# Performance work log

Measured on AMD Instinct MI355X. Metric: run time of the kernel, lower is better.

The kernel has to match this reference:

```python
import jax, jax.numpy as jnp
import numpy as np

N, E, H = 2000, 4096, 256

def setup_inputs() -> dict:
    key = jax.random.key(0)
    ks = jax.random.split(key, 24)
    def rn(k, shape, scale=0.05):
        return jax.random.normal(k, shape, dtype=jnp.float32) * scale
    inp = {
        'x': jax.random.randint(ks[0], (N, 1), 0, 5),
        'pos': rn(ks[1], (N, 3), 1.0),
        'edge_index': jax.random.randint(ks[2], (2, E), 0, N),
        'edge_atr': rn(ks[3], (E, 5), 1.0),
        'emb_table': rn(ks[4], (5, 5), 1.0),
        'lin0_W': rn(ks[5], (H, 8)), 'lin0_b': jnp.zeros((H,), jnp.float32),
        'mlp1_W': rn(ks[6], (128, 5)), 'mlp1_b': jnp.zeros((128,), jnp.float32),
        'mlp2_W': rn(ks[7], (H * H, 128), 0.01), 'mlp2_b': jnp.zeros((H * H,), jnp.float32),
        'conv_b': jnp.zeros((H,), jnp.float32),
        'gru_Wih': rn(ks[8], (3 * H, H)), 'gru_Whh': rn(ks[9], (3 * H, H)),
        'gru_bih': jnp.zeros((3 * H,), jnp.float32), 'gru_bhh': jnp.zeros((3 * H,), jnp.float32),
        'lin1_W': rn(ks[10], (H, 2 * H)), 'lin1_b': jnp.zeros((H,), jnp.float32),
        'lin2_W': rn(ks[11], (242, H)), 'lin2_b': jnp.zeros((242,), jnp.float32),
        'l6_W1': rn(ks[12], (128, 2 * H)), 'l6_b1': jnp.zeros((128,), jnp.float32),
        'bn_g': jnp.ones((128,), jnp.float32), 'bn_b': jnp.zeros((128,), jnp.float32),
        'l6_W2': rn(ks[13], (1, 128)), 'l6_b2': jnp.zeros((1,), jnp.float32),
    }
    return inp

def _gru_step(m, h, Wih, Whh, bih, bhh):
    gi = m @ Wih.T + bih  # [N,3H]
    gh = h @ Whh.T + bhh
    gir, giz, gin = jnp.split(gi, 3, axis=1)
    ghr, ghz, ghn = jnp.split(gh, 3, axis=1)
    r = jax.nn.sigmoid(gir + ghr)
    z = jax.nn.sigmoid(giz + ghz)
    n = jnp.tanh(gin + r * ghn)
    return (1.0 - z) * n + z * h

def reference(x, pos, edge_index, edge_atr, emb_table, lin0_W, lin0_b,
              mlp1_W, mlp1_b, mlp2_W, mlp2_b, conv_b,
              gru_Wih, gru_Whh, gru_bih, gru_bhh,
              lin1_W, lin1_b, lin2_W, lin2_b,
              l6_W1, l6_b1, bn_g, bn_b, l6_W2, l6_b2):
    node_emb = emb_table[x[:, 0]]                      # [N,5]
    in_p = jnp.concatenate([node_emb, pos], axis=1)    # [N,8]
    out = jax.nn.relu(in_p @ lin0_W.T + lin0_b)        # [N,H]
    h = out
    row, col = edge_index[0], edge_index[1]
    # edge-conditioned weights (edge_atr is loop-invariant -> compute once)
    he = jax.nn.relu(edge_atr @ mlp1_W.T + mlp1_b)     # [E,128]
    W_e = (he @ mlp2_W.T + mlp2_b).reshape(E, H, H)    # [E,H,H]
    counts = jnp.clip(jax.ops.segment_sum(jnp.ones((E,), jnp.float32), col, num_segments=N), 1.0)
    for _ in range(3):
        msg = jnp.einsum('eh,eho->eo', out[row], W_e)  # gather + per-edge matmul
        agg = jax.ops.segment_sum(msg, col, num_segments=N) / counts[:, None] + conv_b
        m = jax.nn.relu(agg)
        h = _gru_step(m, h, gru_Wih, gru_Whh, gru_bih, gru_bhh)
        out = h
    out_concat = jnp.concatenate([out[row], out[col]], axis=1)  # [E,2H]
    o1 = jax.nn.relu(out_concat @ lin1_W.T + lin1_b)
    out2 = o1 @ lin2_W.T + lin2_b                       # [E,242]
    # lin6: Linear -> BatchNorm1d (batch stats, training mode) -> ReLU -> Linear
    h1 = out_concat @ l6_W1.T + l6_b1                   # [E,128]
    mu = jnp.mean(h1, axis=0)
    var = jnp.var(h1, axis=0)
    h1n = (h1 - mu) * jax.lax.rsqrt(var + 1e-5) * bn_g + bn_b
    precs = jax.nn.relu(h1n) @ l6_W2.T + l6_b2          # [E,1]
    return (out2, precs)
```

## Files before the change

kernel.cpp:

```cpp
#include <hip/hip_runtime.h>
#include <hip/hip_bf16.h>

constexpr int N_ = 2000;
constexpr int E_ = 4096;
constexpr int H_ = 256;
constexpr int KH_ = 128;
constexpr int NV_ = H_ * KH_;
constexpr int MPAD_ = 2048;
constexpr int NG_ = 768;
constexpr float VSCALE = 64.f;
constexpr float VSCALE_INV = 1.f / 64.f;

typedef short bf16x8 __attribute__((ext_vector_type(8)));
typedef float f32x4  __attribute__((ext_vector_type(4)));
typedef float f32x2  __attribute__((ext_vector_type(2)));

__device__ __forceinline__ float bf_lo(unsigned u) { return __uint_as_float(u << 16); }
__device__ __forceinline__ float bf_hi(unsigned u) { return __uint_as_float(u & 0xffff0000u); }
__device__ __forceinline__ short bfbits(float f) {
    __hip_bfloat16 b = __float2bfloat16(f);
    return *(short*)&b;
}

#define PIPE_WAIT_ENTER(N_OUTST)                                   \
    asm volatile("s_waitcnt vmcnt(" #N_OUTST ")" ::: "memory");    \
    __builtin_amdgcn_s_barrier();                                  \
    asm volatile("" ::: "memory");                                 \
    __builtin_amdgcn_sched_barrier(0);

#define PIPE_EXIT()                                                \
    __builtin_amdgcn_sched_barrier(0);                             \
    asm volatile("" ::: "memory");                                 \
    __builtin_amdgcn_s_barrier();

__global__ void k_lin0(const int* __restrict__ x, const float* __restrict__ pos,
                       const float* __restrict__ emb, const float* __restrict__ W,
                       const float* __restrict__ b, float* __restrict__ out,
                       __hip_bfloat16* __restrict__ Abf) {
    int n = blockIdx.x, t = threadIdx.x;
    if (n >= N_) { Abf[(size_t)n * H_ + t] = __float2bfloat16(0.f); return; }
    __shared__ float in_p[8];
    if (t < 5) in_p[t] = emb[x[n] * 5 + t];
    else if (t < 8) in_p[t] = pos[n * 3 + (t - 5)];
    __syncthreads();
    float acc = b[t];
#pragma unroll
    for (int i = 0; i < 8; i++) acc += in_p[i] * W[t * 8 + i];
    float v = fmaxf(acc, 0.f);
    out[n * H_ + t] = v;
    Abf[(size_t)n * H_ + t] = __float2bfloat16(v);
}

__global__ void k_he(const float* __restrict__ ea, const float* __restrict__ W,
                     const float* __restrict__ b, float* __restrict__ he) {
    int e = blockIdx.x, t = threadIdx.x;
    __shared__ float a[5];
    if (t < 5) a[t] = ea[e * 5 + t];
    __syncthreads();
    float acc = b[t];
#pragma unroll
    for (int i = 0; i < 5; i++) acc += a[i] * W[t * 5 + i];
    he[e * KH_ + t] = fmaxf(acc, 0.f);
}

__global__ void k_counts(const int* __restrict__ ei, float* __restrict__ counts) {
    int e = blockIdx.x * blockDim.x + threadIdx.x;
    if (e < E_) atomicAdd(&counts[ei[E_ + e]], 1.0f);
}

__global__ void k_trans_bt(const float* __restrict__ W, __hip_bfloat16* __restrict__ Bt) {
    __shared__ float tile[32][68];
    int t = threadIdx.x;
    int n0 = blockIdx.x * 64, k0 = blockIdx.y * 32;
#pragma unroll
    for (int i = 0; i < 2; i++) {
        int idx = t + i * 256;
        int kk = idx >> 4, nn = (idx & 15) * 4;
        float4 f = *(const float4*)&W[(size_t)(k0 + kk) * NV_ + n0 + nn];
        *(float4*)&tile[kk][nn] = f;
    }
    __syncthreads();
#pragma unroll
    for (int i = 0; i < 2; i++) {
        int idx = t + i * 256;
        int nn = idx >> 3, k4 = (idx & 7) * 4;
        short4 s;
        s.x = bfbits(tile[k4 + 0][nn]);
        s.y = bfbits(tile[k4 + 1][nn]);
        s.z = bfbits(tile[k4 + 2][nn]);
        s.w = bfbits(tile[k4 + 3][nn]);
        *(short4*)&Bt[(size_t)(n0 + nn) * H_ + k0 + k4] = s;
    }
}

__global__ void k_prep_w(const float* __restrict__ Wih, const float* __restrict__ Whh,
                         const float* __restrict__ lin1W, const float* __restrict__ l6W1,
                         const float* __restrict__ lin2W, const float* __restrict__ b2,
                         __hip_bfloat16* __restrict__ WihB, __hip_bfloat16* __restrict__ WhhB,
                         __hip_bfloat16* __restrict__ Bpk,
                         __hip_bfloat16* __restrict__ lin2Wb, __hip_bfloat16* __restrict__ BtB) {
    int i = blockIdx.x * 256 + threadIdx.x;
    if (i < NG_ * H_) {
        WihB[i] = __float2bfloat16(Wih[i]);
        WhhB[i] = __float2bfloat16(Whh[i]);
    }
    Bpk[i] = __float2bfloat16(i < 256 * 512 ? lin1W[i] : l6W1[i - 256 * 512]);
    if (i < 128 * 2 * H_) {
        int r = i >> 8, k = i & 255;
        lin2Wb[i] = __float2bfloat16(r < 242 ? lin2W[r * H_ + k] : 0.f);
        int o = i >> 8, h = i & 255;
        BtB[o * H_ + h] = __float2bfloat16(b2[h * H_ + o]);
    }
}

template <int KD, bool RELU, bool OUT_BF16>
__global__ __launch_bounds__(256, 3) void k_gemm_nt(const __hip_bfloat16* __restrict__ A,
                                                    const __hip_bfloat16* __restrict__ Bt,
                                                    float* __restrict__ Cf,
                                                    __hip_bfloat16* __restrict__ Cb,
                                                    const float* __restrict__ bias,
                                                    int ldc, int ncols, int mvalid) {
    __shared__ __align__(16) short As[2][4096];
    __shared__ __align__(16) short Bs[2][4096];
    int t = threadIdx.x;
    int lane = t & 63, wave = t >> 6;
    int wm = wave >> 1, wn = wave & 1;
    int quad = lane >> 4, l16 = lane & 15;
    int row0 = blockIdx.y * 128, col0 = blockIdx.x * 128;

    f32x4 acc[4][4] = {};
    int r_ld = (lane >> 2);
    int koff = (((lane & 3) ^ ((lane >> 3) & 3)) * 8);
    int swz = (l16 >> 1) & 3;
    constexpr int NST = KD / 32;

    auto stage = [&](int buf, int k0) {
#pragma unroll
        for (int c = 0; c < 4; c++) {
            int q = wave * 4 + c;
            int ch = q & 7;
            int r = ch * 16 + r_ld;
            const __hip_bfloat16* gp;
            short* lp;
            if (q < 8) { gp = A  + (size_t)(row0 + r) * KD + k0 + koff; lp = &As[buf][ch * 512]; }
            else       { gp = Bt + (size_t)(col0 + r) * KD + k0 + koff; lp = &Bs[buf][ch * 512]; }
            __builtin_amdgcn_global_load_lds(
                (const __attribute__((address_space(1))) unsigned int*)(uintptr_t)gp,
                (__attribute__((address_space(3))) unsigned int*)(uintptr_t)lp,
                16, 0, 0);
        }
    };

    stage(0, 0);
    for (int kk = 0; kk < NST; kk++) {
        int cur = kk & 1;
        if (kk + 1 < NST) {
            stage(cur ^ 1, (kk + 1) * 32);
            PIPE_WAIT_ENTER(4)
        } else {
            PIPE_WAIT_ENTER(0)
        }
        bf16x8 a[4], b[4];
#pragma unroll
        for (int i = 0; i < 4; i++)
            a[i] = *(const bf16x8*)&As[cur][(wm * 64 + i * 16 + l16) * 32 + ((quad ^ swz) << 3)];
#pragma unroll
        for (int j = 0; j < 4; j++)
            b[j] = *(const bf16x8*)&Bs[cur][(wn * 64 + j * 16 + l16) * 32 + ((quad ^ swz) << 3)];
#pragma unroll
        for (int i = 0; i < 4; i++)
#pragma unroll
            for (int j = 0; j < 4; j++)
                acc[i][j] = __builtin_amdgcn_mfma_f32_16x16x32_bf16(a[i], b[j], acc[i][j], 0, 0, 0);
        PIPE_EXIT()
    }

#pragma unroll
    for (int i = 0; i < 4; i++) {
        int gm0 = row0 + wm * 64 + i * 16 + quad * 4;
#pragma unroll
        for (int r = 0; r < 4; r++) {
            int gm = gm0 + r;
            if (gm < mvalid) {
#pragma unroll
                for (int j = 0; j < 4; j++) {
                    int col = col0 + wn * 64 + l16 + j * 16;
                    if (col < ncols) {
                        float v = acc[i][j][r];
                        if (bias) v += bias[col];
                        if (RELU) v = fmaxf(v, 0.f);
                        if (OUT_BF16) Cb[(size_t)gm * ldc + col] = __float2bfloat16(v);
                        else          Cf[(size_t)gm * ldc + col] = v;
                    }
                }
            }
        }
    }
}

__global__ __launch_bounds__(256, 4) void k_gemm_VP(const __hip_bfloat16* __restrict__ Abf,
                                                    const __hip_bfloat16* __restrict__ Bt,
                                                    const __hip_bfloat16* __restrict__ WhhB,
                                                    const __hip_bfloat16* __restrict__ BtB,
                                                    const float* __restrict__ bhh,
                                                    float* __restrict__ gh,
                                                    float* __restrict__ outb,
                                                    unsigned char* __restrict__ V8) {
    __shared__ __align__(16) short As[2][4096];
    __shared__ __align__(16) short Bs[2][4096];
    int bid = blockIdx.x;
    int t = threadIdx.x;
    int lane = t & 63, wave = t >> 6;
    int wm = wave >> 1, wn = wave & 1;
    int quad = lane >> 4, l16 = lane & 15;
    int r_ld = (lane >> 2);
    int koff = (((lane & 3) ^ ((lane >> 3) & 3)) * 8);
    int swz = (l16 >> 1) & 3;

    if (bid < 128) {
        int pbx = bid & 7, pby = bid >> 3;
        bool ob = (pbx >= 6);
        const __hip_bfloat16* Bp = ob ? BtB : WhhB;
        int col0 = ob ? (pbx - 6) * 128 : pbx * 128;
        int ldc = ob ? H_ : NG_;
        float* C = ob ? outb : gh;
        int row0 = pby * 128;

        f32x4 acc[4][4] = {};
        auto stage = [&](int buf, int k0) {
#pragma unroll
            for (int c = 0; c < 4; c++) {
                int q = wave * 4 + c;
                int ch = q & 7;
                int r = ch * 16 + r_ld;
                const __hip_bfloat16* gp;
                short* lp;
                if (q < 8) { gp = Abf + ((size_t)(row0 + r) << 8) + k0 + koff; lp = &As[buf][ch * 512]; }
                else       { gp = Bp  + ((size_t)(col0 + r) << 8) + k0 + koff; lp = &Bs[buf][ch * 512]; }
                __builtin_amdgcn_global_load_lds(
                    (const __attribute__((address_space(1))) unsigned int*)(uintptr_t)gp,
                    (__attribute__((address_space(3))) unsigned int*)(uintptr_t)lp,
                    16, 0, 0);
            }
        };
        stage(0, 0);
        for (int kk = 0; kk < 8; kk++) {
            int cur = kk & 1;
            if (kk + 1 < 8) {
                stage(cur ^ 1, (kk + 1) * 32);
                PIPE_WAIT_ENTER(4)
            } else {
                PIPE_WAIT_ENTER(0)
            }
            bf16x8 a[4], b[4];
#pragma unroll
            for (int i = 0; i < 4; i++)
                a[i] = *(const bf16x8*)&As[cur][(wm * 64 + i * 16 + l16) * 32 + ((quad ^ swz) << 3)];
#pragma unroll
            for (int j = 0; j < 4; j++)
                b[j] = *(const bf16x8*)&Bs[cur][(wn * 64 + j * 16 + l16) * 32 + ((quad ^ swz) << 3)];
#pragma unroll
            for (int i = 0; i < 4; i++)
#pragma unroll
                for (int j = 0; j < 4; j++)
                    acc[i][j] = __builtin_amdgcn_mfma_f32_16x16x32_bf16(a[i], b[j], acc[i][j], 0, 0, 0);
            PIPE_EXIT()
        }
#pragma unroll
        for (int i = 0; i < 4; i++) {
            int gm0 = row0 + wm * 64 + i * 16 + quad * 4;
#pragma unroll
            for (int r = 0; r < 4; r++) {
                int gm = gm0 + r;
                if (gm < N_) {
#pragma unroll
                    for (int j = 0; j < 4; j++) {
                        int col = col0 + wn * 64 + l16 + j * 16;
                        float v = acc[i][j][r] + (ob ? 0.f : bhh[col]);
                        C[(size_t)gm * ldc + col] = v;
                    }
                }
            }
        }
        return;
    }

    int vb = bid - 128;
    int bx = vb & 255, by = vb >> 8;
    int row0 = by * 128, col0 = bx * 128;
    int obase = bx * 8;
    int kb = (bx >> 5) * 16;
    short* Ps = &As[0][0];

    f32x4 acc[4][4] = {};
    auto stage = [&](int buf, int k0) {
#pragma unroll
        for (int c = 0; c < 4; c++) {
            int q = wave * 4 + c;
            int ch = q & 7;
            const __hip_bfloat16* gp;
            short* lp;
            if (q < 8) {
                gp = Abf + ((size_t)(row0 + ch * 16 + r_ld) << 8) + k0 + koff;
                lp = &As[buf][ch * 512];
            } else {
                int nv = ((obase + ch) & 255) * 128 + kb + r_ld;
                gp = Bt + ((size_t)nv << 8) + k0 + koff;
                lp = &Bs[buf][ch * 512];
            }
            __builtin_amdgcn_global_load_lds(
                (const __attribute__((address_space(1))) unsigned int*)(uintptr_t)gp,
                (__attribute__((address_space(3))) unsigned int*)(uintptr_t)lp,
                16, 0, 0);
        }
    };
    stage(0, 0);
    for (int kk = 0; kk < 8; kk++) {
        int cur = kk & 1;
        if (kk + 1 < 8) {
            stage(cur ^ 1, (kk + 1) * 32);
            PIPE_WAIT_ENTER(4)
        } else {
            PIPE_WAIT_ENTER(0)
        }
        bf16x8 a[4], b[4];
#pragma unroll
        for (int i = 0; i < 4; i++)
            a[i] = *(const bf16x8*)&As[cur][(wm * 64 + i * 16 + l16) * 32 + ((quad ^ swz) << 3)];
#pragma unroll
        for (int j = 0; j < 4; j++)
            b[j] = *(const bf16x8*)&Bs[cur][(wn * 64 + j * 16 + l16) * 32 + ((quad ^ swz) << 3)];
#pragma unroll
        for (int i = 0; i < 4; i++)
#pragma unroll
            for (int j = 0; j < 4; j++)
                acc[i][j] = __builtin_amdgcn_mfma_f32_16x16x32_bf16(a[i], b[j], acc[i][j], 0, 0, 0);
        PIPE_EXIT()
    }

#pragma unroll
    for (int pp = 0; pp < 4; pp++) {
        if (wm == (pp >> 1)) {
#pragma unroll
            for (int ii = 0; ii < 2; ii++) {
                const int i = (pp & 1) * 2 + ii;
                int lr = ii * 16 + quad * 4;
#pragma unroll
                for (int r = 0; r < 4; r++) {
#pragma unroll
                    for (int j = 0; j < 4; j++) {
                        int col = wn * 64 + j * 16 + l16;
                        Ps[(lr + r) * 136 + col] = bfbits(acc[i][j][r] * VSCALE);
                    }
                }
            }
        }
        __syncthreads();
        {
            int row = t >> 3;
            int col = (t & 7) * 16;
            int gm = row0 + pp * 32 + row;
            if (gm < N_) {
                uint4 ua = *(const uint4*)&Ps[row * 136 + col];
                uint4 ub = *(const uint4*)&Ps[row * 136 + col + 8];
                unsigned p0 = __builtin_amdgcn_cvt_pk_fp8_f32(bf_lo(ua.x), bf_hi(ua.x), 0, false);
                p0 = __builtin_amdgcn_cvt_pk_fp8_f32(bf_lo(ua.y), bf_hi(ua.y), p0, true);
                unsigned p1 = __builtin_amdgcn_cvt_pk_fp8_f32(bf_lo(ua.z), bf_hi(ua.z), 0, false);
                p1 = __builtin_amdgcn_cvt_pk_fp8_f32(bf_lo(ua.w), bf_hi(ua.w), p1, true);
                unsigned p2 = __builtin_amdgcn_cvt_pk_fp8_f32(bf_lo(ub.x), bf_hi(ub.x), 0, false);
                p2 = __builtin_amdgcn_cvt_pk_fp8_f32(bf_lo(ub.y), bf_hi(ub.y), p2, true);
                unsigned p3 = __builtin_amdgcn_cvt_pk_fp8_f32(bf_lo(ub.z), bf_hi(ub.z), 0, false);
                p3 = __builtin_amdgcn_cvt_pk_fp8_f32(bf_lo(ub.w), bf_hi(ub.w), p3, true);
                uint4 o4;
                o4.x = p0; o4.y = p1; o4.z = p2; o4.w = p3;
                *(uint4*)(V8 + (size_t)gm * NV_ + col0 + col) = o4;
            }
        }
        __syncthreads();
    }
}

__global__ __launch_bounds__(256, 3) void k_gemm_gi(const float* __restrict__ agg,
                                                    const float* __restrict__ counts,
                                                    const float* __restrict__ conv_b,
                                                    const __hip_bfloat16* __restrict__ WihB,
                                                    const float* __restrict__ bih,
                                                    float* __restrict__ gi) {
    __shared__ __align__(16) short As[2][4096];
    __shared__ __align__(16) short Bs[2][4096];
    __shared__ __align__(16) float conv_lds[256];
    int t = threadIdx.x;
    int lane = t & 63, wave = t >> 6;
    int wm = wave >> 1, wn = wave & 1;
    int quad = lane >> 4, l16 = lane & 15;
    int row0 = blockIdx.y * 128, col0 = blockIdx.x * 128;
    int r_ld = (lane >> 2);
    int koff = (((lane & 3) ^ ((lane >> 3) & 3)) * 8);
    int swz = (l16 >> 1) & 3;
    bool arole = (wave < 2);

    conv_lds[t] = conv_b[t];
    __syncthreads();

    f32x4 acc[4][4] = {};
    float rcv[4];
    const float* asrc[4];
    if (arole) {
#pragma unroll
        for (int c = 0; c < 4; c++) {
            int ch = wave * 4 + c;
            int row = row0 + ch * 16 + r_ld;
            int rowc = row < N_ ? row : N_ - 1;
            rcv[c] = 1.f / fmaxf(counts[rowc], 1.f);
            asrc[c] = agg + (size_t)rowc * 256;
        }
    }
    float4 R[2][4][2];

    auto loadA = [&](int buf, int k0) {
#pragma unroll
        for (int c = 0; c < 4; c++) {
            R[buf][c][0] = *(const float4*)(asrc[c] + k0 + koff);
            R[buf][c][1] = *(const float4*)(asrc[c] + k0 + koff + 4);
        }
    };
    auto stageB = [&](int buf, int k0) {
#pragma unroll
        for (int c = 0; c < 4; c++) {
            int ch = (wave * 4 + c) & 7;
            const __hip_bfloat16* gp = WihB + (size_t)(col0 + ch * 16 + r_ld) * 256 + k0 + koff;
            short* lp = &Bs[buf][ch * 512];
            __builtin_amdgcn_global_load_lds(
                (const __attribute__((address_space(1))) unsigned int*)(uintptr_t)gp,
                (__attribute__((address_space(3))) unsigned int*)(uintptr_t)lp,
                16, 0, 0);
        }
    };
    auto writeA = [&](int buf, int k0) {
        float4 cb0 = *(const float4*)&conv_lds[k0 + koff];
        float4 cb1 = *(const float4*)&conv_lds[k0 + koff + 4];
#pragma unroll
        for (int c = 0; c < 4; c++) {
            int ch = wave * 4 + c;
            float rc = rcv[c];
            float4 a0 = R[buf][c][0], a1 = R[buf][c][1];
            bf16x8 v;
            v[0] = bfbits(fmaxf(a0.x * rc + cb0.x, 0.f));
            v[1] = bfbits(fmaxf(a0.y * rc + cb0.y, 0.f));
            v[2] = bfbits(fmaxf(a0.z * rc + cb0.z, 0.f));
            v[3] = bfbits(fmaxf(a0.w * rc + cb0.w, 0.f));
            v[4] = bfbits(fmaxf(a1.x * rc + cb1.x, 0.f));
            v[5] = bfbits(fmaxf(a1.y * rc + cb1.y, 0.f));
            v[6] = bfbits(fmaxf(a1.z * rc + cb1.z, 0.f));
            v[7] = bfbits(fmaxf(a1.w * rc + cb1.w, 0.f));
            *(bf16x8*)&As[buf][ch * 512 + lane * 8] = v;
        }
    };

    if (arole) loadA(0, 0); else stageB(0, 0);
#pragma unroll
    for (int kk = 0; kk < 8; kk++) {
        const int cur = kk & 1;
        if (kk + 1 < 8) {
            if (arole) loadA(cur ^ 1, (kk + 1) * 32);
            else       stageB(cur ^ 1, (kk + 1) * 32);
        }
        if (arole) {
            writeA(cur, kk * 32);
            asm volatile("s_waitcnt lgkmcnt(0)" ::: "memory");
        } else {
            if (kk + 1 < 8) { asm volatile("s_waitcnt vmcnt(4)" ::: "memory"); }
            else            { asm volatile("s_waitcnt vmcnt(0)" ::: "memory"); }
        }
        __builtin_amdgcn_s_barrier();
        asm volatile("" ::: "memory");
        __builtin_amdgcn_sched_barrier(0);
        bf16x8 a[4], b[4];
#pragma unroll
        for (int i = 0; i < 4; i++)
            a[i] = *(const bf16x8*)&As[cur][(wm * 64 + i * 16 + l16) * 32 + ((quad ^ swz) << 3)];
#pragma unroll
        for (int j = 0; j < 4; j++)
            b[j] = *(const bf16x8*)&Bs[cur][(wn * 64 + j * 16 + l16) * 32 + ((quad ^ swz) << 3)];
#pragma unroll
        for (int i = 0; i < 4; i++)
#pragma unroll
            for (int j = 0; j < 4; j++)
                acc[i][j] = __builtin_amdgcn_mfma_f32_16x16x32_bf16(a[i], b[j], acc[i][j], 0, 0, 0);
        PIPE_EXIT()
    }

#pragma unroll
    for (int i = 0; i < 4; i++) {
        int gm0 = row0 + wm * 64 + i * 16 + quad * 4;
#pragma unroll
        for (int r = 0; r < 4; r++) {
            int gm = gm0 + r;
            if (gm < N_) {
#pragma unroll
                for (int j = 0; j < 4; j++) {
                    int col = col0 + wn * 64 + l16 + j * 16;
                    gi[(size_t)gm * NG_ + col] = acc[i][j][r] + bih[col];
                }
            }
        }
    }
}

__global__ __launch_bounds__(256, 3) void k_gemm_tail2(const int* __restrict__ ei,
                                                       const float* __restrict__ h,
                                                       const __hip_bfloat16* __restrict__ Bpk,
                                                       const float* __restrict__ b1,
                                                       const float* __restrict__ b2,
                                                       __hip_bfloat16* __restrict__ o1bf,
                                                       float* __restrict__ h1) {
    __shared__ __align__(16) short As[2][4096];
    __shared__ __align__(16) short Bs[2][4096];
    int t = threadIdx.x;
    int lane = t & 63, wave = t >> 6;
    int wm = wave >> 1, wn = wave & 1;
    int quad = lane >> 4, l16 = lane & 15;
    int row0 = blockIdx.y * 128, col0 = blockIdx.x * 128;
    int r_ld = (lane >> 2);
    int koff = (((lane & 3) ^ ((lane >> 3) & 3)) * 8);
    int swz = (l16 >> 1) & 3;
    bool arole = (wave < 2);

    f32x4 acc[4][4] = {};
    const float* src0[4];
    const float* src1[4];
    if (arole) {
#pragma unroll
        for (int c = 0; c < 4; c++) {
            int ch = wave * 4 + c;
            int e = row0 + ch * 16 + r_ld;
            src0[c] = h + (size_t)ei[e] * 256;
            src1[c] = h + (size_t)ei[E_ + e] * 256;
        }
    }
    float4 R[2][4][2];

    auto loadA = [&](int buf, int k0) {
        bool hi = (k0 >= 256);
        int kc = (k0 & 255) + koff;
#pragma unroll
        for (int c = 0; c < 4; c++) {
            const float* s = hi ? src1[c] : src0[c];
            R[buf][c][0] = *(const float4*)(s + kc);
            R[buf][c][1] = *(const float4*)(s + kc + 4);
        }
    };
    auto stageB = [&](int buf, int k0) {
#pragma unroll
        for (int c = 0; c < 4; c++) {
            int ch = (wave * 4 + c) & 7;
            const __hip_bfloat16* gp = Bpk + (size_t)(col0 + ch * 16 + r_ld) * 512 + k0 + koff;
            short* lp = &Bs[buf][ch * 512];
            __builtin_amdgcn_global_load_lds(
                (const __attribute__((address_space(1))) unsigned int*)(uintptr_t)gp,
                (__attribute__((address_space(3))) unsigned int*)(uintptr_t)lp,
                16, 0, 0);
        }
    };
    auto writeA = [&](int buf) {
#pragma unroll
        for (int c = 0; c < 4; c++) {
            int ch = wave * 4 + c;
            float4 a0 = R[buf][c][0], a1 = R[buf][c][1];
            bf16x8 v;
            v[0] = bfbits(a0.x); v[1] = bfbits(a0.y); v[2] = bfbits(a0.z); v[3] = bfbits(a0.w);
            v[4] = bfbits(a1.x); v[5] = bfbits(a1.y); v[6] = bfbits(a1.z); v[7] = bfbits(a1.w);
            *(bf16x8*)&As[buf][ch * 512 + lane * 8] = v;
        }
    };

    if (arole) loadA(0, 0); else stageB(0, 0);
#pragma unroll
    for (int kk = 0; kk < 16; kk++) {
        const int cur = kk & 1;
        if (kk + 1 < 16) {
            if (arole) loadA(cur ^ 1, (kk + 1) * 32);
            else       stageB(cur ^ 1, (kk + 1) * 32);
        }
        if (arole) {
            writeA(cur);
            asm volatile("s_waitcnt lgkmcnt(0)" ::: "memory");
        } else {
            if (kk + 1 < 16) { asm volatile("s_waitcnt vmcnt(4)" ::: "memory"); }
            else             { asm volatile("s_waitcnt vmcnt(0)" ::: "memory"); }
        }
        __builtin_amdgcn_s_barrier();
        asm volatile("" ::: "memory");
        __builtin_amdgcn_sched_barrier(0);
        bf16x8 a[4], b[4];
#pragma unroll
        for (int i = 0; i < 4; i++)
            a[i] = *(const bf16x8*)&As[cur][(wm * 64 + i * 16 + l16) * 32 + ((quad ^ swz) << 3)];
#pragma unroll
        for (int j = 0; j < 4; j++)
            b[j] = *(const bf16x8*)&Bs[cur][(wn * 64 + j * 16 + l16) * 32 + ((quad ^ swz) << 3)];
#pragma unroll
        for (int i = 0; i < 4; i++)
#pragma unroll
            for (int j = 0; j < 4; j++)
                acc[i][j] = __builtin_amdgcn_mfma_f32_16x16x32_bf16(a[i], b[j], acc[i][j], 0, 0, 0);
        PIPE_EXIT()
    }

#pragma unroll
    for (int i = 0; i < 4; i++) {
        int gm0 = row0 + wm * 64 + i * 16 + quad * 4;
#pragma unroll
        for (int r = 0; r < 4; r++) {
            int gm = gm0 + r;
#pragma unroll
            for (int j = 0; j < 4; j++) {
                int col = col0 + wn * 64 + l16 + j * 16;
                float v = acc[i][j][r];
                if (col < 256) {
                    v = fmaxf(v + b1[col], 0.f);
                    o1bf[(size_t)gm * H_ + col] = __float2bfloat16(v);
                } else {
                    h1[(size_t)gm * 128 + (col - 256)] = v + b2[col - 256];
                }
            }
        }
    }
}

__global__ void k_msg(const int* __restrict__ ei, const float* __restrict__ he,
                      const unsigned char* __restrict__ V8, const float* __restrict__ outb,
                      float* __restrict__ agg) {
    int e = blockIdx.x, o = threadIdx.x;
    __shared__ float hs[KH_];
    if (o < KH_) hs[o] = he[e * KH_ + o] * VSCALE_INV;
    __syncthreads();
    int r = ei[e], c = ei[E_ + e];
    float acc = outb[(size_t)r * H_ + o];
    const unsigned char* vbase = V8 + (size_t)r * NV_ + o * 16;
#pragma unroll
    for (int q = 0; q < 8; q++) {
        uint4 u = *(const uint4*)(vbase + (size_t)q * 4096);
        const float* hp = hs + q * 16;
        f32x2 f;
        f = __builtin_amdgcn_cvt_pk_f32_fp8(u.x, false); acc += hp[0]  * f.x + hp[1]  * f.y;
        f = __builtin_amdgcn_cvt_pk_f32_fp8(u.x, true);  acc += hp[2]  * f.x + hp[3]  * f.y;
        f = __builtin_amdgcn_cvt_pk_f32_fp8(u.y, false); acc += hp[4]  * f.x + hp[5]  * f.y;
        f = __builtin_amdgcn_cvt_pk_f32_fp8(u.y, true);  acc += hp[6]  * f.x + hp[7]  * f.y;
        f = __builtin_amdgcn_cvt_pk_f32_fp8(u.z, false); acc += hp[8]  * f.x + hp[9]  * f.y;
        f = __builtin_amdgcn_cvt_pk_f32_fp8(u.z, true);  acc += hp[10] * f.x + hp[11] * f.y;
        f = __builtin_amdgcn_cvt_pk_f32_fp8(u.w, false); acc += hp[12] * f.x + hp[13] * f.y;
        f = __builtin_amdgcn_cvt_pk_f32_fp8(u.w, true);  acc += hp[14] * f.x + hp[15] * f.y;
    }
    atomicAdd(&agg[(size_t)c * H_ + o], acc);
}

__global__ void k_gru_update(const float* __restrict__ gi, const float* __restrict__ gh,
                             float* __restrict__ h, __hip_bfloat16* __restrict__ Abf,
                             float* __restrict__ agg) {
    int i = blockIdx.x * blockDim.x + threadIdx.x;
    if (i >= N_ * H_) return;
    int n = i >> 8, j = i & 255;
    const float* gip = gi + (size_t)n * NG_;
    const float* ghp = gh + (size_t)n * NG_;
    float r = 1.f / (1.f + expf(-(gip[j] + ghp[j])));
    float z = 1.f / (1.f + expf(-(gip[H_ + j] + ghp[H_ + j])));
    float nn = tanhf(gip[2 * H_ + j] + r * ghp[2 * H_ + j]);
    float hv = (1.f - z) * nn + z * h[i];
    h[i] = hv;
    Abf[i] = __float2bfloat16(hv);
    agg[i] = 0.f;
}

__global__ void k_bnstats(const float* __restrict__ h1, float* __restrict__ mu,
                          float* __restrict__ rsig) {
    int j = blockIdx.x, t = threadIdx.x;
    float s = 0.f, ss = 0.f;
    for (int e = t; e < E_; e += 256) {
        float v = h1[(size_t)e * 128 + j];
        s += v;
        ss += v * v;
    }
    __shared__ float rs[256], rss[256];
    rs[t] = s; rss[t] = ss;
    __syncthreads();
    for (int off = 128; off > 0; off >>= 1) {
        if (t < off) { rs[t] += rs[t + off]; rss[t] += rss[t + off]; }
        __syncthreads();
    }
    if (t == 0) {
        float m_ = rs[0] / E_;
        float v_ = rss[0] / E_ - m_ * m_;
        mu[j] = m_;
        rsig[j] = rsqrtf(v_ + 1e-5f);
    }
}

__global__ void k_precs(const float* __restrict__ h1, const float* __restrict__ mu,
                        const float* __restrict__ rsig, const float* __restrict__ g,
                        const float* __restrict__ bb, const float* __restrict__ W2,
                        const float* __restrict__ b2, float* __restrict__ out) {
    int e = blockIdx.x * blockDim.x + threadIdx.x;
    if (e >= E_) return;
    float acc = b2[0];
#pragma unroll 4
    for (int j = 0; j < 128; j++) {
        float v = (h1[(size_t)e * 128 + j] - mu[j]) * rsig[j] * g[j] + bb[j];
        acc += fmaxf(v, 0.f) * W2[j];
    }
    out[(size_t)E_ * 242 + e] = acc;
}

extern "C" void kernel_launch(void* const* d_in, const int* in_sizes, int n_in,
                              void* d_out, int out_size, void* d_ws, size_t ws_size,
                              hipStream_t stream) {
    const int*   x        = (const int*)  d_in[0];
    const float* pos      = (const float*)d_in[1];
    const int*   ei       = (const int*)  d_in[2];
    const float* edge_atr = (const float*)d_in[3];
    const float* emb      = (const float*)d_in[4];
    const float* lin0_W   = (const float*)d_in[5];
    const float* lin0_b   = (const float*)d_in[6];
    const float* mlp1_W   = (const float*)d_in[7];
    const float* mlp1_b   = (const float*)d_in[8];
    const float* mlp2_W   = (const float*)d_in[9];
    const float* mlp2_b   = (const float*)d_in[10];
    const float* conv_b   = (const float*)d_in[11];
    const float* gru_Wih  = (const float*)d_in[12];
    const float* gru_Whh  = (const float*)d_in[13];
    const float* gru_bih  = (const float*)d_in[14];
    const float* gru_bhh  = (const float*)d_in[15];
    const float* lin1_W   = (const float*)d_in[16];
    const float* lin1_b   = (const float*)d_in[17];
    const float* lin2_W   = (const float*)d_in[18];
    const float* lin2_b   = (const float*)d_in[19];
    const float* l6_W1    = (const float*)d_in[20];
    const float* l6_b1    = (const float*)d_in[21];
    const float* bn_g     = (const float*)d_in[22];
    const float* bn_b     = (const float*)d_in[23];
    const float* l6_W2    = (const float*)d_in[24];
    const float* l6_b2    = (const float*)d_in[25];
    float* out = (float*)d_out;

    char* w = (char*)d_ws;
    size_t off = 0;
    auto alloc = [&](size_t bytes) -> void* {
        void* p = w + off;
        off = (off + bytes + 255) & ~(size_t)255;
        return p;
    };
    float* hbuf   = (float*)alloc((size_t)N_ * H_ * 4);
    float* aggm   = (float*)alloc((size_t)N_ * H_ * 4);
    float* outb   = (float*)alloc((size_t)N_ * H_ * 4);
    float* he     = (float*)alloc((size_t)E_ * KH_ * 4);
    float* gi     = (float*)alloc((size_t)N_ * NG_ * 4);
    float* gh     = (float*)alloc((size_t)N_ * NG_ * 4);
    float* h1     = (float*)alloc((size_t)E_ * 128 * 4);
    float* counts = (float*)alloc((size_t)N_ * 4);
    float* mu     = (float*)alloc(128 * 4);
    float* rsig   = (float*)alloc(128 * 4);
    unsigned char* V8      = (unsigned char*)alloc((size_t)N_ * NV_);
    __hip_bfloat16* Abf    = (__hip_bfloat16*)alloc((size_t)MPAD_ * H_ * 2);
    __hip_bfloat16* Bt     = (__hip_bfloat16*)alloc((size_t)NV_ * H_ * 2);
    __hip_bfloat16* WihB   = (__hip_bfloat16*)alloc((size_t)NG_ * H_ * 2);
    __hip_bfloat16* WhhB   = (__hip_bfloat16*)alloc((size_t)NG_ * H_ * 2);
    __hip_bfloat16* Bpk    = (__hip_bfloat16*)alloc((size_t)384 * 512 * 2);
    __hip_bfloat16* lin2Wb = (__hip_bfloat16*)alloc((size_t)H_ * H_ * 2);
    __hip_bfloat16* BtB    = (__hip_bfloat16*)alloc((size_t)H_ * H_ * 2);
    __hip_bfloat16* o1bf   = (__hip_bfloat16*)alloc((size_t)E_ * H_ * 2);

    k_lin0<<<MPAD_, 256, 0, stream>>>(x, pos, emb, lin0_W, lin0_b, hbuf, Abf);
    k_he<<<E_, 128, 0, stream>>>(edge_atr, mlp1_W, mlp1_b, he);
    hipMemsetAsync(counts, 0, (size_t)N_ * 4, stream);
    hipMemsetAsync(aggm, 0, (size_t)N_ * H_ * 4, stream);
    k_counts<<<(E_ + 255) / 256, 256, 0, stream>>>(ei, counts);
    k_trans_bt<<<dim3(NV_ / 64, H_ / 32), 256, 0, stream>>>(mlp2_W, Bt);
    k_prep_w<<<768, 256, 0, stream>>>(gru_Wih, gru_Whh, lin1_W, l6_W1, lin2_W, mlp2_b,
                                      WihB, WhhB, Bpk, lin2Wb, BtB);

    for (int it = 0; it < 3; it++) {
        k_gemm_VP<<<128 + (NV_ / 128) * (MPAD_ / 128), 256, 0, stream>>>(
            Abf, Bt, WhhB, BtB, gru_bhh, gh, outb, V8);
        k_msg<<<E_, 256, 0, stream>>>(ei, he, V8, outb, aggm);
        k_gemm_gi<<<dim3(6, MPAD_ / 128), 256, 0, stream>>>(
            aggm, counts, conv_b, WihB, gru_bih, gi);
        k_gru_update<<<(N_ * H_ + 255) / 256, 256, 0, stream>>>(gi, gh, hbuf, Abf, aggm);
    }

    k_gemm_tail2<<<dim3(3, E_ / 128), 256, 0, stream>>>(ei, hbuf, Bpk, lin1_b, l6_b1,
                                                        o1bf, h1);
    k_gemm_nt<256, false, false><<<dim3(2, E_ / 128), 256, 0, stream>>>(
        o1bf, lin2Wb, out, nullptr, lin2_b, 242, 242, E_);
    k_bnstats<<<128, 256, 0, stream>>>(h1, mu, rsig);
    k_precs<<<(E_ + 255) / 256, 256, 0, stream>>>(h1, mu, rsig, bn_g, bn_b, l6_W2, l6_b2, out);
}
```

Measured before the change: 494.3 us.

## Drop warp-specialized A/B staging in GI and tail GEMMs; materialize concat buffer

In the GRU input GEMM, every wave now both loads and converts its share of the fp32 A tile and issues async global-to-LDS loads for B, where before two waves handled A and two handled B. The tail GEMM no longer gathers and converts rows itself. A new k_concat kernel first writes the gathered [row, col] hidden states to a bf16 buffer, and the GEMM then stages both A and B through direct global-to-LDS loads. This is meant to balance load work across waves and simplify the tail pipeline, at the cost of an extra kernel launch and an extra round trip through global memory for the concatenated edge features.

```diff
diff --git a/kernel.cpp b/kernel.cpp
--- a/kernel.cpp
+++ b/kernel.cpp
@@ -111,6 +111,14 @@
         int o = i >> 8, h = i & 255;
         BtB[o * H_ + h] = __float2bfloat16(b2[h * H_ + o]);
     }
+}
+
+__global__ void k_concat(const int* __restrict__ ei, const float* __restrict__ h,
+                         __hip_bfloat16* __restrict__ Cbf) {
+    int e = blockIdx.x, t = threadIdx.x;
+    int r = ei[e], c = ei[E_ + e];
+    Cbf[(size_t)e * 512 + t]       = __float2bfloat16(h[(size_t)r * H_ + t]);
+    Cbf[(size_t)e * 512 + 256 + t] = __float2bfloat16(h[(size_t)c * H_ + t]);
 }
 
 template <int KD, bool RELU, bool OUT_BF16>
@@ -397,37 +405,34 @@
     int r_ld = (lane >> 2);
     int koff = (((lane & 3) ^ ((lane >> 3) & 3)) * 8);
     int swz = (l16 >> 1) & 3;
-    bool arole = (wave < 2);
 
     conv_lds[t] = conv_b[t];
     __syncthreads();
 
     f32x4 acc[4][4] = {};
-    float rcv[4];
-    const float* asrc[4];
-    if (arole) {
-#pragma unroll
-        for (int c = 0; c < 4; c++) {
-            int ch = wave * 4 + c;
-            int row = row0 + ch * 16 + r_ld;
-            int rowc = row < N_ ? row : N_ - 1;
-            rcv[c] = 1.f / fmaxf(counts[rowc], 1.f);
-            asrc[c] = agg + (size_t)rowc * 256;
-        }
-    }
-    float4 R[2][4][2];
+    float rcv[2];
+    const float* asrc[2];
+#pragma unroll
+    for (int c = 0; c < 2; c++) {
+        int ch = wave * 2 + c;
+        int row = row0 + ch * 16 + r_ld;
+        int rowc = row < N_ ? row : N_ - 1;
+        rcv[c] = 1.f / fmaxf(counts[rowc], 1.f);
+        asrc[c] = agg + (size_t)rowc * 256;
+    }
+    float4 R[2][2][2];
 
     auto loadA = [&](int buf, int k0) {
 #pragma unroll
-        for (int c = 0; c < 4; c++) {
+        for (int c = 0; c < 2; c++) {
             R[buf][c][0] = *(const float4*)(asrc[c] + k0 + koff);
             R[buf][c][1] = *(const float4*)(asrc[c] + k0 + koff + 4);
         }
     };
     auto stageB = [&](int buf, int k0) {
 #pragma unroll
-        for (int c = 0; c < 4; c++) {
-            int ch = (wave * 4 + c) & 7;
+        for (int c = 0; c < 2; c++) {
+            int ch = wave * 2 + c;
             const __hip_bfloat16* gp = WihB + (size_t)(col0 + ch * 16 + r_ld) * 256 + k0 + koff;
             short* lp = &Bs[buf][ch * 512];
             __builtin_amdgcn_global_load_lds(
@@ -440,8 +445,8 @@
         float4 cb0 = *(const float4*)&conv_lds[k0 + koff];
         float4 cb1 = *(const float4*)&conv_lds[k0 + koff + 4];
 #pragma unroll
-        for (int c = 0; c < 4; c++) {
-            int ch = wave * 4 + c;
+        for (int c = 0; c < 2; c++) {
+            int ch = wave * 2 + c;
             float rc = rcv[c];
             float4 a0 = R[buf][c][0], a1 = R[buf][c][1];
             bf16x8 v;
@@ -457,21 +462,19 @@
         }
     };
 
-    if (arole) loadA(0, 0); else stageB(0, 0);
+    loadA(0, 0);
+    stageB(0, 0);
 #pragma unroll
     for (int kk = 0; kk < 8; kk++) {
         const int cur = kk & 1;
         if (kk + 1 < 8) {
-            if (arole) loadA(cur ^ 1, (kk + 1) * 32);
-            else       stageB(cur ^ 1, (kk + 1) * 32);
-        }
-        if (arole) {
-            writeA(cur, kk * 32);
-            asm volatile("s_waitcnt lgkmcnt(0)" ::: "memory");
-        } else {
-            if (kk + 1 < 8) { asm volatile("s_waitcnt vmcnt(4)" ::: "memory"); }
-            else            { asm volatile("s_waitcnt vmcnt(0)" ::: "memory"); }
-        }
+            loadA(cur ^ 1, (kk + 1) * 32);
+            stageB(cur ^ 1, (kk + 1) * 32);
+        }
+        writeA(cur, kk * 32);
+        if (kk + 1 < 8) { asm volatile("s_waitcnt vmcnt(6)" ::: "memory"); }
+        else            { asm volatile("s_waitcnt vmcnt(0)" ::: "memory"); }
+        asm volatile("s_waitcnt lgkmcnt(0)" ::: "memory");
         __builtin_amdgcn_s_barrier();
         asm volatile("" ::: "memory");
         __builtin_amdgcn_sched_barrier(0);
@@ -507,13 +510,12 @@
     }
 }
 
-__global__ __launch_bounds__(256, 3) void k_gemm_tail2(const int* __restrict__ ei,
-                                                       const float* __restrict__ h,
-                                                       const __hip_bfloat16* __restrict__ Bpk,
-                                                       const float* __restrict__ b1,
-                                                       const float* __restrict__ b2,
-                                                       __hip_bfloat16* __restrict__ o1bf,
-                                                       float* __restrict__ h1) {
+__global__ __launch_bounds__(256, 3) void k_gemm_tail(const __hip_bfloat16* __restrict__ A,
+                                                      const __hip_bfloat16* __restrict__ Bpk,
+                                                      const float* __restrict__ b1,
+                                                      const float* __restrict__ b2,
+                                                      __hip_bfloat16* __restrict__ o1bf,
+                                                      float* __restrict__ h1) {
     __shared__ __align__(16) short As[2][4096];
     __shared__ __align__(16) short Bs[2][4096];
     int t = threadIdx.x;
@@ -521,77 +523,38 @@
     int wm = wave >> 1, wn = wave & 1;
     int quad = lane >> 4, l16 = lane & 15;
     int row0 = blockIdx.y * 128, col0 = blockIdx.x * 128;
+
+    f32x4 acc[4][4] = {};
     int r_ld = (lane >> 2);
     int koff = (((lane & 3) ^ ((lane >> 3) & 3)) * 8);
     int swz = (l16 >> 1) & 3;
-    bool arole = (wave < 2);
-
-    f32x4 acc[4][4] = {};
-    const float* src0[4];
-    const float* src1[4];
-    if (arole) {
+
+    auto stage = [&](int buf, int k0) {
 #pragma unroll
         for (int c = 0; c < 4; c++) {
-            int ch = wave * 4 + c;
-            int e = row0 + ch * 16 + r_ld;
-            src0[c] = h + (size_t)ei[e] * 256;
-            src1[c] = h + (size_t)ei[E_ + e] * 256;
-        }
-    }
-    float4 R[2][4][2];
-
-    auto loadA = [&](int buf, int k0) {
-        bool hi = (k0 >= 256);
-        int kc = (k0 & 255) + koff;
-#pragma unroll
-        for (int c = 0; c < 4; c++) {
-            const float* s = hi ? src1[c] : src0[c];
-            R[buf][c][0] = *(const float4*)(s + kc);
-            R[buf][c][1] = *(const float4*)(s + kc + 4);
-        }
-    };
-    auto stageB = [&](int buf, int k0) {
-#pragma unroll
-        for (int c = 0; c < 4; c++) {
-            int ch = (wave * 4 + c) & 7;
-            const __hip_bfloat16* gp = Bpk + (size_t)(col0 + ch * 16 + r_ld) * 512 + k0 + koff;
-            short* lp = &Bs[buf][ch * 512];
+            int q = wave * 4 + c;
+            int ch = q & 7;
+            int r = ch * 16 + r_ld;
+            const __hip_bfloat16* gp;
+            short* lp;
+            if (q < 8) { gp = A   + (size_t)(row0 + r) * 512 + k0 + koff; lp = &As[buf][ch * 512]; }
+            else       { gp = Bpk + (size_t)(col0 + r) * 512 + k0 + koff; lp = &Bs[buf][ch * 512]; }
             __builtin_amdgcn_global_load_lds(
                 (const __attribute__((address_space(1))) unsigned int*)(uintptr_t)gp,
                 (__attribute__((address_space(3))) unsigned int*)(uintptr_t)lp,
                 16, 0, 0);
         }
     };
-    auto writeA = [&](int buf) {
-#pragma unroll
-        for (int c = 0; c < 4; c++) {
-            int ch = wave * 4 + c;
-            float4 a0 = R[buf][c][0], a1 = R[buf][c][1];
-            bf16x8 v;
-            v[0] = bfbits(a0.x); v[1] = bfbits(a0.y); v[2] = bfbits(a0.z); v[3] = bfbits(a0.w);
-            v[4] = bfbits(a1.x); v[5] = bfbits(a1.y); v[6] = bfbits(a1.z); v[7] = bfbits(a1.w);
-            *(bf16x8*)&As[buf][ch * 512 + lane * 8] = v;
-        }
-    };
-
-    if (arole) loadA(0, 0); else stageB(0, 0);
-#pragma unroll
+
+    stage(0, 0);
     for (int kk = 0; kk < 16; kk++) {
-        const int cur = kk & 1;
+        int cur = kk & 1;
         if (kk + 1 < 16) {
-            if (arole) loadA(cur ^ 1, (kk + 1) * 32);
-            else       stageB(cur ^ 1, (kk + 1) * 32);
-        }
-        if (arole) {
-            writeA(cur);
-            asm volatile("s_waitcnt lgkmcnt(0)" ::: "memory");
+            stage(cur ^ 1, (kk + 1) * 32);
+            PIPE_WAIT_ENTER(4)
         } else {
-            if (kk + 1 < 16) { asm volatile("s_waitcnt vmcnt(4)" ::: "memory"); }
-            else             { asm volatile("s_waitcnt vmcnt(0)" ::: "memory"); }
-        }
-        __builtin_amdgcn_s_barrier();
-        asm volatile("" ::: "memory");
-        __builtin_amdgcn_sched_barrier(0);
+            PIPE_WAIT_ENTER(0)
+        }
         bf16x8 a[4], b[4];
 #pragma unroll
         for (int i = 0; i < 4; i++)
@@ -767,6 +730,7 @@
     __hip_bfloat16* Bpk    = (__hip_bfloat16*)alloc((size_t)384 * 512 * 2);
     __hip_bfloat16* lin2Wb = (__hip_bfloat16*)alloc((size_t)H_ * H_ * 2);
     __hip_bfloat16* BtB    = (__hip_bfloat16*)alloc((size_t)H_ * H_ * 2);
+    __hip_bfloat16* Cbf    = (__hip_bfloat16*)alloc((size_t)E_ * 2 * H_ * 2);
     __hip_bfloat16* o1bf   = (__hip_bfloat16*)alloc((size_t)E_ * H_ * 2);
 
     k_lin0<<<MPAD_, 256, 0, stream>>>(x, pos, emb, lin0_W, lin0_b, hbuf, Abf);
@@ -787,8 +751,8 @@
         k_gru_update<<<(N_ * H_ + 255) / 256, 256, 0, stream>>>(gi, gh, hbuf, Abf, aggm);
     }
 
-    k_gemm_tail2<<<dim3(3, E_ / 128), 256, 0, stream>>>(ei, hbuf, Bpk, lin1_b, l6_b1,
-                                                        o1bf, h1);
+    k_concat<<<E_, 256, 0, stream>>>(ei, hbuf, Cbf);
+    k_gemm_tail<<<dim3(3, E_ / 128), 256, 0, stream>>>(Cbf, Bpk, lin1_b, l6_b1, o1bf, h1);
     k_gemm_nt<256, false, false><<<dim3(2, E_ / 128), 256, 0, stream>>>(
         o1bf, lin2Wb, out, nullptr, lin2_b, 242, 242, E_);
     k_bnstats<<<128, 256, 0, stream>>>(h1, mu, rsig);
```

After: 446.7 us. -9.6%, faster.
